# Kernel optimization log

Hardware: AMD Instinct MI355X
Metric: run time of the kernel (lower is better)

Reference implementation:

```python
import jax, jax.numpy as jnp
import numpy as np

DROPOUT_P = 0.5  # used as an additive constant in the normalizers, not as dropout
N = 384


def setup_inputs() -> dict:
    key = jax.random.key(0)
    k1, k2 = jax.random.split(key)
    inp = jax.random.uniform(k1, (N, N, N), dtype=jnp.float32)
    w = jax.random.uniform(k2, (N, N, N), dtype=jnp.float32)
    return {"input": inp, "w": w}


def reference(input, w):
    # e[i,j,l] = sum_k input[i,j,k] * w[l,k,j]
    e = jnp.einsum('ijk,lkj->ijl', input, w)
    # k (normalized by input row-sums) is dead code in the original forward;
    # only q and v feed the output, so we skip it.
    v = e  # second identical einsum in the source
    s_in = input.sum(axis=-1, keepdims=True)          # [N, N, 1]
    # einsum('ijk,ijl->ijl', input, w) == (sum_k input) * w
    q = s_in * w
    q = q / (DROPOUT_P + w.sum(axis=-1, keepdims=True))
    # causal mask: strict upper triangle set to -inf, broadcast over batch
    mask = jnp.triu(jnp.full((N, N), -jnp.inf, dtype=q.dtype), k=1)  # [N, N]
    attn = jax.nn.softmax(q + mask[None, :, :], axis=-1)              # [N, N, N]
    return jnp.matmul(attn, v)
```

## Files before the change

kernel.cpp:

```cpp
#include <hip/hip_runtime.h>
#include <hip/hip_bf16.h>


#define N 384
#define N2 (N * N)
#define BK 64
static const size_t N3 = (size_t)N * N * N;

typedef __attribute__((ext_vector_type(8))) short s16x8;
typedef __attribute__((ext_vector_type(4))) float f32x4;

#define AS1 __attribute__((address_space(1)))
#define AS3 __attribute__((address_space(3)))
__device__ __forceinline__ void gll16(const void* g, void* l) {
    __builtin_amdgcn_global_load_lds((const AS1 unsigned int*)g,
                                     (AS3 unsigned int*)l, 16, 0, 0);
}

__device__ __forceinline__ unsigned short f32_to_bf16(float f) {
    unsigned int u = __float_as_uint(f);
    u += 0x7FFFu + ((u >> 16) & 1u);
    return (unsigned short)(u >> 16);
}
__device__ __forceinline__ float bf16_to_f32(unsigned short h) {
    return __uint_as_float((unsigned int)h << 16);
}
__device__ __forceinline__ unsigned int pk2(float a, float b) {
    return (unsigned int)f32_to_bf16(a) | ((unsigned int)f32_to_bf16(b) << 16);
}

__global__ __launch_bounds__(256) void kT(const float* __restrict__ w,
                                          unsigned short* __restrict__ wt) {
    __shared__ unsigned short tile[64][68];
    const int r0 = blockIdx.x * 64;
    const int j0 = blockIdx.y * 64;
    const int tx = threadIdx.x & 63;
    const int ty = threadIdx.x >> 6;
#pragma unroll
    for (int p = 0; p < 16; ++p) {
        const int r = ty * 16 + p;
        tile[r][tx] = f32_to_bf16(w[(size_t)(r0 + r) * N + j0 + tx]);
    }
    __syncthreads();
#pragma unroll
    for (int p = 0; p < 16; ++p) {
        const int jj = ty * 16 + p;
        wt[(size_t)(j0 + jj) * N2 + r0 + tx] = tile[tx][jj];
    }
}

__global__ __launch_bounds__(256, 4) void k_e2(const float* __restrict__ in,
                                               const unsigned short* __restrict__ wt,
                                               unsigned short* __restrict__ e) {
    __shared__ union {
        struct { unsigned short A[64 * 64]; unsigned short B[192 * 64]; } s;
        unsigned short C[64 * 200];
    } sm;

    const int lin = blockIdx.x;
    const int swz = (lin & 7) * 576 + (lin >> 3);
    const int j   = swz / 12;
    const int sub = swz % 12;
    const int i0  = (sub >> 1) * 64;
    const int l0  = (sub & 1) * 192;

    const int t = threadIdx.x, lane = t & 63, wv = t >> 6;
    const int fr = lane & 15, fx = lane >> 4;

    const int ra = t >> 2, ca = (t & 3) * 2;
    const float* Ab = in + (size_t)(i0 + ra) * N2 + (size_t)j * N + ca * 8;
    unsigned short* AsW0 = sm.s.A + ra * 64 + (((ca + 0) ^ (ra & 7)) * 8);
    unsigned short* AsW1 = sm.s.A + ra * 64 + (((ca + 1) ^ (ra & 7)) * 8);

    const unsigned short* Wj = wt + (size_t)j * N2 + (size_t)l0 * N;
    const int rb_off = lane >> 3;
    const int p8     = lane & 7;

    f32x4 acc[4][3];
#pragma unroll
    for (int m = 0; m < 4; ++m)
#pragma unroll
        for (int n = 0; n < 3; ++n) acc[m][n] = (f32x4){0.f, 0.f, 0.f, 0.f};

    float4 va[4];
    va[0] = *(const float4*)(Ab);
    va[1] = *(const float4*)(Ab + 4);
    va[2] = *(const float4*)(Ab + 8);
    va[3] = *(const float4*)(Ab + 12);

    for (int k0 = 0; k0 < N; k0 += BK) {
        __syncthreads();
        {
            uint4 a0, a1;
            a0.x = pk2(va[0].x, va[0].y); a0.y = pk2(va[0].z, va[0].w);
            a0.z = pk2(va[1].x, va[1].y); a0.w = pk2(va[1].z, va[1].w);
            a1.x = pk2(va[2].x, va[2].y); a1.y = pk2(va[2].z, va[2].w);
            a1.z = pk2(va[3].x, va[3].y); a1.w = pk2(va[3].z, va[3].w);
            *(uint4*)AsW0 = a0;
            *(uint4*)AsW1 = a1;
        }
#pragma unroll
        for (int itb = 0; itb < 6; ++itb) {
            const int rb = wv * 48 + itb * 8 + rb_off;
            const int sc = p8 ^ (rb & 7);
            gll16(Wj + (size_t)rb * N + k0 + sc * 8,
                  sm.s.B + (wv * 48 + itb * 8) * 64);
        }
        if (k0 + BK < N) {
            const float* An = Ab + k0 + BK;
            va[0] = *(const float4*)(An);
            va[1] = *(const float4*)(An + 4);
            va[2] = *(const float4*)(An + 8);
            va[3] = *(const float4*)(An + 12);
        }
        __syncthreads();
#pragma unroll
        for (int kk = 0; kk < 2; ++kk) {
            s16x8 af[4], bf[3];
#pragma unroll
            for (int m = 0; m < 4; ++m) {
                const int row = m * 16 + fr;
                const int x   = (kk * 4 + fx) ^ (row & 7);
                af[m] = *(const s16x8*)(sm.s.A + row * 64 + x * 8);
            }
#pragma unroll
            for (int n = 0; n < 3; ++n) {
                const int row = wv * 48 + n * 16 + fr;
                const int x   = (kk * 4 + fx) ^ (row & 7);
                bf[n] = *(const s16x8*)(sm.s.B + row * 64 + x * 8);
            }
#pragma unroll
            for (int m = 0; m < 4; ++m)
#pragma unroll
                for (int n = 0; n < 3; ++n)
                    acc[m][n] = __builtin_amdgcn_mfma_f32_16x16x32_bf16(
                        af[m], bf[n], acc[m][n], 0, 0, 0);
        }
    }

    __syncthreads();
#pragma unroll
    for (int m = 0; m < 4; ++m)
#pragma unroll
        for (int n = 0; n < 3; ++n)
#pragma unroll
            for (int r = 0; r < 4; ++r)
                sm.C[(m * 16 + fx * 4 + r) * 200 + wv * 48 + n * 16 + fr] =
                    f32_to_bf16(acc[m][n][r]);
    __syncthreads();
#pragma unroll
    for (int it = 0; it < 6; ++it) {
        const int cid = it * 256 + t;
        const int row = cid / 24;
        const int c   = cid % 24;
        *(uint4*)(e + (size_t)(i0 + row) * N2 + (size_t)j * N + l0 + c * 8) =
            *(const uint4*)&sm.C[row * 200 + c * 8];
    }
}

__global__ __launch_bounds__(256) void k_eT(const unsigned short* __restrict__ e,
                                            unsigned short* __restrict__ et) {
    __shared__ unsigned short tile[64][68];
    const int m0 = blockIdx.x * 64, l0 = blockIdx.y * 64;
    const size_t ib = (size_t)blockIdx.z * N2;
    const int t  = threadIdx.x;
    const int c4 = (t & 15) * 4, r = t >> 4;
#pragma unroll
    for (int p = 0; p < 4; ++p) {
        ushort4 v = *(const ushort4*)(e + ib + (size_t)(m0 + r + 16 * p) * N + l0 + c4);
        tile[c4 + 0][r + 16 * p] = v.x;
        tile[c4 + 1][r + 16 * p] = v.y;
        tile[c4 + 2][r + 16 * p] = v.z;
        tile[c4 + 3][r + 16 * p] = v.w;
    }
    __syncthreads();
#pragma unroll
    for (int p = 0; p < 4; ++p) {
        const int lr = r + 16 * p;
        ushort4 v = *(const ushort4*)&tile[lr][c4];
        *(ushort4*)(et + ib + (size_t)(l0 + lr) * N + m0 + c4) = v;
    }
}

__global__ __launch_bounds__(256) void k_attn(const float* __restrict__ in,
                                              const float* __restrict__ w,
                                              unsigned short* __restrict__ attn) {
    const int row  = blockIdx.x * 4 + (threadIdx.x >> 6);
    const int lane = threadIdx.x & 63;
    const int jr   = row % N;

    const float2* ip = (const float2*)(in + (size_t)row * N);
    const float2* wp = (const float2*)(w + (size_t)row * N);

    float2 wv[3];
    float rs_in = 0.f, rs_w = 0.f;
#pragma unroll
    for (int c = 0; c < 3; ++c) {
        float2 iv = ip[lane + 64 * c];
        wv[c] = wp[lane + 64 * c];
        rs_in += iv.x + iv.y;
        rs_w  += wv[c].x + wv[c].y;
    }
#pragma unroll
    for (int s = 1; s < 64; s <<= 1) {
        rs_in += __shfl_xor(rs_in, s, 64);
        rs_w  += __shfl_xor(rs_w, s, 64);
    }
    const float scale = rs_in / (0.5f + rs_w);

    float2 q[3];
    float mx = -INFINITY;
#pragma unroll
    for (int c = 0; c < 3; ++c) {
        const int l = (lane + 64 * c) * 2;
        q[c].x = (l     <= jr) ? scale * wv[c].x : -INFINITY;
        q[c].y = (l + 1 <= jr) ? scale * wv[c].y : -INFINITY;
        mx = fmaxf(mx, fmaxf(q[c].x, q[c].y));
    }
#pragma unroll
    for (int s = 1; s < 64; s <<= 1) mx = fmaxf(mx, __shfl_xor(mx, s, 64));

    float2 p[3];
    float sum = 0.f;
#pragma unroll
    for (int c = 0; c < 3; ++c) {
        const int l = (lane + 64 * c) * 2;
        p[c].x = (l     <= jr) ? exp2f((q[c].x - mx) * 1.44269504f) : 0.f;
        p[c].y = (l + 1 <= jr) ? exp2f((q[c].y - mx) * 1.44269504f) : 0.f;
        sum += p[c].x + p[c].y;
    }
#pragma unroll
    for (int s = 1; s < 64; s <<= 1) sum += __shfl_xor(sum, s, 64);
    const float inv = 1.f / sum;
    unsigned int* ap = (unsigned int*)(attn + (size_t)row * N);
#pragma unroll
    for (int c = 0; c < 3; ++c)
        ap[lane + 64 * c] = pk2(p[c].x * inv, p[c].y * inv);
}

__global__ __launch_bounds__(256, 4) void k_av2(const unsigned short* __restrict__ attn,
                                                const unsigned short* __restrict__ et,
                                                float* __restrict__ out) {
    __shared__ union {
        struct { unsigned short A[64 * 64]; unsigned short B[192 * 64]; } s;
        float C[32 * 196];
    } sm;

    const int lin = blockIdx.x;
    const int swz = (lin & 7) * 576 + (lin >> 3);
    const int i   = swz / 12;
    const int sub = swz % 12;
    const int j0  = (sub >> 1) * 64;
    const int l0  = (sub & 1) * 192;
    const int kmax = j0 + 64;

    const int t = threadIdx.x, lane = t & 63, wv = t >> 6;
    const int fr = lane & 15, fx = lane >> 4;
    const int rb_off = lane >> 3;
    const int p8     = lane & 7;

    const unsigned short* Ag = attn + (size_t)i * N2 + (size_t)j0 * N;
    const unsigned short* Bg = et + (size_t)i * N2 + (size_t)l0 * N;

    f32x4 acc[4][3];
#pragma unroll
    for (int m = 0; m < 4; ++m)
#pragma unroll
        for (int n = 0; n < 3; ++n) acc[m][n] = (f32x4){0.f, 0.f, 0.f, 0.f};

    for (int k0 = 0; k0 < kmax; k0 += BK) {
        __syncthreads();
#pragma unroll
        for (int ita = 0; ita < 2; ++ita) {
            const int rb = wv * 16 + ita * 8 + rb_off;
            const int sc = p8 ^ (rb & 7);
            gll16(Ag + (size_t)rb * N + k0 + sc * 8,
                  sm.s.A + (wv * 16 + ita * 8) * 64);
        }
#pragma unroll
        for (int itb = 0; itb < 6; ++itb) {
            const int rb = wv * 48 + itb * 8 + rb_off;
            const int sc = p8 ^ (rb & 7);
            gll16(Bg + (size_t)rb * N + k0 + sc * 8,
                  sm.s.B + (wv * 48 + itb * 8) * 64);
        }
        __syncthreads();
#pragma unroll
        for (int kk = 0; kk < 2; ++kk) {
            s16x8 af[4], bf[3];
#pragma unroll
            for (int m = 0; m < 4; ++m) {
                const int row = m * 16 + fr;
                const int x   = (kk * 4 + fx) ^ (row & 7);
                af[m] = *(const s16x8*)(sm.s.A + row * 64 + x * 8);
            }
#pragma unroll
            for (int n = 0; n < 3; ++n) {
                const int row = wv * 48 + n * 16 + fr;
                const int x   = (kk * 4 + fx) ^ (row & 7);
                bf[n] = *(const s16x8*)(sm.s.B + row * 64 + x * 8);
            }
#pragma unroll
            for (int m = 0; m < 4; ++m)
#pragma unroll
                for (int n = 0; n < 3; ++n)
                    acc[m][n] = __builtin_amdgcn_mfma_f32_16x16x32_bf16(
                        af[m], bf[n], acc[m][n], 0, 0, 0);
        }
    }

#pragma unroll
    for (int ph = 0; ph < 2; ++ph) {
        __syncthreads();
#pragma unroll
        for (int mm = 0; mm < 2; ++mm)
#pragma unroll
            for (int n = 0; n < 3; ++n)
#pragma unroll
                for (int r = 0; r < 4; ++r)
                    sm.C[(mm * 16 + fx * 4 + r) * 196 + wv * 48 + n * 16 + fr] =
                        acc[ph * 2 + mm][n][r];
        __syncthreads();
#pragma unroll
        for (int it = 0; it < 6; ++it) {
            const int cid = it * 256 + t;
            const int row = cid / 48;
            const int c   = cid % 48;
            *(float4*)(out + (size_t)i * N2 + (size_t)(j0 + ph * 32 + row) * N + l0 + c * 4) =
                *(const float4*)&sm.C[row * 196 + c * 4];
        }
    }
}

extern "C" void kernel_launch(void* const* d_in, const int* in_sizes, int n_in,
                              void* d_out, int out_size, void* d_ws, size_t ws_size,
                              hipStream_t stream) {
    const float* in = (const float*)d_in[0];
    const float* w  = (const float*)d_in[1];
    float* out      = (float*)d_out;

    unsigned short* r0 = (unsigned short*)d_ws;
    unsigned short* r1 = (unsigned short*)d_ws + N3;

    kT<<<dim3(N2 / 64, N / 64), 256, 0, stream>>>(w, r0);
    k_e2<<<dim3(4608), 256, 0, stream>>>(in, r0, r1);
    k_eT<<<dim3(6, 6, N), 256, 0, stream>>>(r1, r0);
    k_attn<<<dim3(N2 / 4), 256, 0, stream>>>(in, w, r1);
    k_av2<<<dim3(4608), 256, 0, stream>>>(r1, r0, out);
}
```

Baseline: 435.4 us.

## Fuse causal softmax attention computation into the e-einsum GEMM kernel

Removes the separate softmax kernel. The input row sums come from the A-tile values the GEMM already loads, and blocks with l0==0 compute the masked softmax over w rows, writing bf16 attn to a new third workspace buffer. This saves one launch and one re-read of the input tensor. The cost is that w is read three times per row inside half of the GEMM blocks, which may unbalance the grid, and the workspace now needs three N^3 bf16 buffers. A barrier in the av epilogue was also moved.

```diff
diff --git a/kernel.cpp b/kernel.cpp
--- a/kernel.cpp
+++ b/kernel.cpp
@@ -21,9 +21,6 @@
     unsigned int u = __float_as_uint(f);
     u += 0x7FFFu + ((u >> 16) & 1u);
     return (unsigned short)(u >> 16);
-}
-__device__ __forceinline__ float bf16_to_f32(unsigned short h) {
-    return __uint_as_float((unsigned int)h << 16);
 }
 __device__ __forceinline__ unsigned int pk2(float a, float b) {
     return (unsigned int)f32_to_bf16(a) | ((unsigned int)f32_to_bf16(b) << 16);
@@ -49,9 +46,11 @@
     }
 }
 
-__global__ __launch_bounds__(256, 4) void k_e2(const float* __restrict__ in,
-                                               const unsigned short* __restrict__ wt,
-                                               unsigned short* __restrict__ e) {
+__global__ __launch_bounds__(256, 4) void k_e2f(const float* __restrict__ in,
+                                                const float* __restrict__ w,
+                                                const unsigned short* __restrict__ wt,
+                                                unsigned short* __restrict__ e,
+                                                unsigned short* __restrict__ attn) {
     __shared__ union {
         struct { unsigned short A[64 * 64]; unsigned short B[192 * 64]; } s;
         unsigned short C[64 * 200];
@@ -82,6 +81,8 @@
 #pragma unroll
         for (int n = 0; n < 3; ++n) acc[m][n] = (f32x4){0.f, 0.f, 0.f, 0.f};
 
+    float rsum = 0.f;
+
     float4 va[4];
     va[0] = *(const float4*)(Ab);
     va[1] = *(const float4*)(Ab + 4);
@@ -91,6 +92,10 @@
     for (int k0 = 0; k0 < N; k0 += BK) {
         __syncthreads();
         {
+            rsum += (va[0].x + va[0].y + va[0].z + va[0].w) +
+                    (va[1].x + va[1].y + va[1].z + va[1].w) +
+                    (va[2].x + va[2].y + va[2].z + va[2].w) +
+                    (va[3].x + va[3].y + va[3].z + va[3].w);
             uint4 a0, a1;
             a0.x = pk2(va[0].x, va[0].y); a0.y = pk2(va[0].z, va[0].w);
             a0.z = pk2(va[1].x, va[1].y); a0.w = pk2(va[1].z, va[1].w);
@@ -138,6 +143,9 @@
         }
     }
 
+    rsum += __shfl_xor(rsum, 1, 64);
+    rsum += __shfl_xor(rsum, 2, 64);
+
     __syncthreads();
 #pragma unroll
     for (int m = 0; m < 4; ++m)
@@ -155,6 +163,58 @@
         const int c   = cid % 24;
         *(uint4*)(e + (size_t)(i0 + row) * N2 + (size_t)j * N + l0 + c * 8) =
             *(const uint4*)&sm.C[row * 200 + c * 8];
+    }
+
+    if (l0 == 0) {
+        const int q0 = t & 3;
+        const float* Wrow = w + ((size_t)(i0 + ra) * N + j) * N;
+
+        float s_w = 0.f, mx = -INFINITY;
+#pragma unroll
+        for (int c = 0; c < 24; ++c) {
+            const int col = q0 * 4 + c * 16;
+            float4 v = *(const float4*)(Wrow + col);
+            s_w += v.x + v.y + v.z + v.w;
+            float m0 = (col + 0 <= j) ? v.x : -INFINITY;
+            float m1 = (col + 1 <= j) ? v.y : -INFINITY;
+            float m2 = (col + 2 <= j) ? v.z : -INFINITY;
+            float m3 = (col + 3 <= j) ? v.w : -INFINITY;
+            mx = fmaxf(mx, fmaxf(fmaxf(m0, m1), fmaxf(m2, m3)));
+        }
+        s_w += __shfl_xor(s_w, 1, 64);
+        s_w += __shfl_xor(s_w, 2, 64);
+        mx = fmaxf(mx, __shfl_xor(mx, 1, 64));
+        mx = fmaxf(mx, __shfl_xor(mx, 2, 64));
+
+        const float aa = (rsum / (0.5f + s_w)) * 1.44269504f;
+
+        float s_e = 0.f;
+#pragma unroll
+        for (int c = 0; c < 24; ++c) {
+            const int col = q0 * 4 + c * 16;
+            float4 v = *(const float4*)(Wrow + col);
+            float e0 = (col + 0 <= j) ? exp2f(aa * (v.x - mx)) : 0.f;
+            float e1 = (col + 1 <= j) ? exp2f(aa * (v.y - mx)) : 0.f;
+            float e2 = (col + 2 <= j) ? exp2f(aa * (v.z - mx)) : 0.f;
+            float e3 = (col + 3 <= j) ? exp2f(aa * (v.w - mx)) : 0.f;
+            s_e += e0 + e1 + e2 + e3;
+        }
+        s_e += __shfl_xor(s_e, 1, 64);
+        s_e += __shfl_xor(s_e, 2, 64);
+        const float inv = 1.f / s_e;
+
+        unsigned int* Arow = (unsigned int*)(attn + ((size_t)(i0 + ra) * N + j) * N);
+#pragma unroll
+        for (int c = 0; c < 24; ++c) {
+            const int col = q0 * 4 + c * 16;
+            float4 v = *(const float4*)(Wrow + col);
+            float p0 = (col + 0 <= j) ? exp2f(aa * (v.x - mx)) * inv : 0.f;
+            float p1 = (col + 1 <= j) ? exp2f(aa * (v.y - mx)) * inv : 0.f;
+            float p2 = (col + 2 <= j) ? exp2f(aa * (v.z - mx)) * inv : 0.f;
+            float p3 = (col + 3 <= j) ? exp2f(aa * (v.w - mx)) * inv : 0.f;
+            Arow[col / 2]     = pk2(p0, p1);
+            Arow[col / 2 + 1] = pk2(p2, p3);
+        }
     }
 }
 
@@ -182,62 +242,6 @@
     }
 }
 
-__global__ __launch_bounds__(256) void k_attn(const float* __restrict__ in,
-                                              const float* __restrict__ w,
-                                              unsigned short* __restrict__ attn) {
-    const int row  = blockIdx.x * 4 + (threadIdx.x >> 6);
-    const int lane = threadIdx.x & 63;
-    const int jr   = row % N;
-
-    const float2* ip = (const float2*)(in + (size_t)row * N);
-    const float2* wp = (const float2*)(w + (size_t)row * N);
-
-    float2 wv[3];
-    float rs_in = 0.f, rs_w = 0.f;
-#pragma unroll
-    for (int c = 0; c < 3; ++c) {
-        float2 iv = ip[lane + 64 * c];
-        wv[c] = wp[lane + 64 * c];
-        rs_in += iv.x + iv.y;
-        rs_w  += wv[c].x + wv[c].y;
-    }
-#pragma unroll
-    for (int s = 1; s < 64; s <<= 1) {
-        rs_in += __shfl_xor(rs_in, s, 64);
-        rs_w  += __shfl_xor(rs_w, s, 64);
-    }
-    const float scale = rs_in / (0.5f + rs_w);
-
-    float2 q[3];
-    float mx = -INFINITY;
-#pragma unroll
-    for (int c = 0; c < 3; ++c) {
-        const int l = (lane + 64 * c) * 2;
-        q[c].x = (l     <= jr) ? scale * wv[c].x : -INFINITY;
-        q[c].y = (l + 1 <= jr) ? scale * wv[c].y : -INFINITY;
-        mx = fmaxf(mx, fmaxf(q[c].x, q[c].y));
-    }
-#pragma unroll
-    for (int s = 1; s < 64; s <<= 1) mx = fmaxf(mx, __shfl_xor(mx, s, 64));
-
-    float2 p[3];
-    float sum = 0.f;
-#pragma unroll
-    for (int c = 0; c < 3; ++c) {
-        const int l = (lane + 64 * c) * 2;
-        p[c].x = (l     <= jr) ? exp2f((q[c].x - mx) * 1.44269504f) : 0.f;
-        p[c].y = (l + 1 <= jr) ? exp2f((q[c].y - mx) * 1.44269504f) : 0.f;
-        sum += p[c].x + p[c].y;
-    }
-#pragma unroll
-    for (int s = 1; s < 64; s <<= 1) sum += __shfl_xor(sum, s, 64);
-    const float inv = 1.f / sum;
-    unsigned int* ap = (unsigned int*)(attn + (size_t)row * N);
-#pragma unroll
-    for (int c = 0; c < 3; ++c)
-        ap[lane + 64 * c] = pk2(p[c].x * inv, p[c].y * inv);
-}
-
 __global__ __launch_bounds__(256, 4) void k_av2(const unsigned short* __restrict__ attn,
                                                 const unsigned short* __restrict__ et,
                                                 float* __restrict__ out) {
@@ -309,9 +313,9 @@
         }
     }
 
+    __syncthreads();
 #pragma unroll
     for (int ph = 0; ph < 2; ++ph) {
-        __syncthreads();
 #pragma unroll
         for (int mm = 0; mm < 2; ++mm)
 #pragma unroll
@@ -329,6 +333,7 @@
             *(float4*)(out + (size_t)i * N2 + (size_t)(j0 + ph * 32 + row) * N + l0 + c * 4) =
                 *(const float4*)&sm.C[row * 196 + c * 4];
         }
+        if (ph == 0) __syncthreads();
     }
 }
 
@@ -341,10 +346,10 @@
 
     unsigned short* r0 = (unsigned short*)d_ws;
     unsigned short* r1 = (unsigned short*)d_ws + N3;
+    unsigned short* attn = (unsigned short*)d_ws + 2 * N3;
 
     kT<<<dim3(N2 / 64, N / 64), 256, 0, stream>>>(w, r0);
-    k_e2<<<dim3(4608), 256, 0, stream>>>(in, r0, r1);
+    k_e2f<<<dim3(4608), 256, 0, stream>>>(in, w, r0, r1, attn);
     k_eT<<<dim3(6, 6, N), 256, 0, stream>>>(r1, r0);
-    k_attn<<<dim3(N2 / 4), 256, 0, stream>>>(in, w, r1);
-    k_av2<<<dim3(4608), 256, 0, stream>>>(r1, r0, out);
-}
+    k_av2<<<dim3(4608), 256, 0, stream>>>(attn, r0, out);
+}
```

After: 637.3 us. 1.46x slower.
